# Optimization experiments

Hardware: AMD Instinct MI355X
Metric: run time of the kernel (lower is better)

Reference implementation:

```python
import jax, jax.numpy as jnp
import numpy as np

THRESH = 0.3
DECAY = 0.5


def spike_fn(x):
    # Heaviside threshold (forward only)
    return (x > THRESH).astype(x.dtype)


def setup_inputs() -> dict:
    key = jax.random.key(0)
    k_in, k0, k1, k2 = jax.random.split(key, 4)
    B, D0, T = 128, 512, 512
    inputs = jax.random.uniform(k_in, (B, D0, T), dtype=jnp.float32)
    w0 = jax.random.normal(k0, (512, 1024), dtype=jnp.float32)
    w1 = jax.random.normal(k1, (1024, 1024), dtype=jnp.float32)
    w2 = jax.random.normal(k2, (1024, 512), dtype=jnp.float32)
    return {"inputs": inputs, "w0": w0, "w1": w1, "w2": w2}


def reference(inputs, w0, w1, w2):
    ws = (w0, w1, w2)
    B = inputs.shape[0]
    layer_dims = tuple(w.shape[1] for w in ws)

    # time-major: [T, B, D0]
    xs = jnp.transpose(inputs, (2, 0, 1))

    mem0 = tuple(jnp.zeros((B, d), dtype=inputs.dtype) for d in layer_dims)
    spk0 = tuple(jnp.zeros((B, d), dtype=inputs.dtype) for d in layer_dims)

    def step(carry, x_t):
        mems, spikes = carry
        prev_spike = x_t  # layer-0 spikes come straight from the input
        new_mems, new_spikes = [], []
        for i, w in enumerate(ws):
            # leaky integrate with reset-by-spike, then fire
            mem = mems[i] * DECAY * (1.0 - spikes[i]) + prev_spike @ w
            s = spike_fn(mem)
            new_mems.append(mem)
            new_spikes.append(s)
            prev_spike = s
        return (tuple(new_mems), tuple(new_spikes)), None

    (_, spikes_final), _ = jax.lax.scan(step, (mem0, spk0), xs)
    return spikes_final[-1]
```

## Files before the change

kernel.cpp:

```cpp
#include <hip/hip_runtime.h>


typedef __bf16 bf16;
typedef __attribute__((ext_vector_type(8))) __bf16 bf16x8;
typedef __attribute__((ext_vector_type(16))) float f32x16;
typedef unsigned long long u64;

#define B_   128
#define D0_  512
#define T_   512
#define TS_  128
#define N1_  1024
#define N2_  1024
#define N3_  512
#define MFMA32(a,b,c) __builtin_amdgcn_mfma_f32_32x32x16_bf16((a),(b),(c),0,0,0)

#define GL2LDS(g, l) __builtin_amdgcn_global_load_lds( \
    (const __attribute__((address_space(1))) void*)(g), \
    (__attribute__((address_space(3))) void*)(l), 16, 0, 0)

#define WAIT_BARRIER() do { \
    asm volatile("s_waitcnt vmcnt(0)" ::: "memory"); \
    __builtin_amdgcn_s_barrier(); } while (0)


__global__ __launch_bounds__(256)
void split_w(const float* __restrict__ W, bf16* __restrict__ WTh, bf16* __restrict__ WTl,
             int K, int N)
{
    __shared__ float tile[32][33];
    const int k0 = blockIdx.x * 32, n0 = blockIdx.y * 32;
    const int tx = threadIdx.x & 31, ty = threadIdx.x >> 5;
#pragma unroll
    for (int r = 0; r < 4; ++r)
        tile[ty + r * 8][tx] = W[(size_t)(k0 + ty + r * 8) * N + n0 + tx];
    __syncthreads();
#pragma unroll
    for (int r = 0; r < 4; ++r) {
        int nl = ty + r * 8;
        float v = tile[tx][nl];
        bf16 h = (bf16)v;
        size_t o = (size_t)(n0 + nl) * K + k0 + tx;
        WTh[o] = h;
        WTl[o] = (bf16)(v - (float)h);
    }
}

__global__ __launch_bounds__(256)
void split_x(const float* __restrict__ in, bf16* __restrict__ Xh, bf16* __restrict__ Xl)
{
    __shared__ float tile[32][33];
    const int b = blockIdx.z, d0 = blockIdx.x * 32, t0 = blockIdx.y * 32;
    const int tx = threadIdx.x & 31, ty = threadIdx.x >> 5;
#pragma unroll
    for (int r = 0; r < 4; ++r)
        tile[ty + r * 8][tx] = in[((size_t)b * D0_ + d0 + ty + r * 8) * T_ + t0 + tx];
    __syncthreads();
    const int s = t0 >> 7;
#pragma unroll
    for (int r = 0; r < 4; ++r) {
        int t  = t0 + ty + r * 8;
        int tl = t & (TS_ - 1);
        float v = tile[tx][ty + r * 8];
        bf16 h = (bf16)v;
        size_t o = (((size_t)s * B_ + b) * TS_ + tl) * D0_ + d0 + tx;
        Xh[o] = h;
        Xl[o] = (bf16)(v - (float)h);
    }
}

__device__ __forceinline__ bf16x8 expand8(unsigned v)
{
    union { unsigned u[4]; bf16x8 h; } r;
    const unsigned p = v * 0x8001u;
#pragma unroll
    for (int i = 0; i < 4; ++i)
        r.u[i] = ((p >> (2 * i)) & 0x10001u) * 0x3F80u;
    return r.h;
}

__global__ __launch_bounds__(256, 2)
void snn_layer0(const bf16* __restrict__ Ah, const bf16* __restrict__ Al,
                const bf16* __restrict__ WTh, const bf16* __restrict__ WTl,
                u64* __restrict__ bitsOut)
{
    constexpr int K = D0_;
    __shared__ char smem[65536];
    bf16* sA0  = (bf16*)(smem);
    bf16* sAl0 = (bf16*)(smem + 8192);
    bf16* sB0  = (bf16*)(smem + 16384);
    bf16* sBl0 = (bf16*)(smem + 24576);
    bf16* sA1  = (bf16*)(smem + 32768);
    bf16* sAl1 = (bf16*)(smem + 40960);
    bf16* sB1  = (bf16*)(smem + 49152);
    bf16* sBl1 = (bf16*)(smem + 57344);
    float* If  = (float*)smem;

    const int tid = threadIdx.x, lane = tid & 63, w = tid >> 6;
    const int wm = w & 1, wn = w >> 1;
    const int l31 = lane & 31, kh = lane >> 5;
    const int b = blockIdx.x;
    const int nb = blockIdx.y * 128;

    const int i4 = lane >> 2, c4 = lane & 3;
    const int csrc = c4 ^ ((i4 >> 1) & 3);
    const bf16* gBh = WTh + (size_t)(nb + w * 32 + i4) * K + csrc * 8;
    const bf16* gBl = WTl + (size_t)(nb + w * 32 + i4) * K + csrc * 8;
    const int wT = w * 32 * 32;

    int rA[2], rB[2], swA[2], swB[2];
#pragma unroll
    for (int i = 0; i < 2; ++i) {
        rA[i] = wm * 64 + i * 32 + l31;
        rB[i] = wn * 64 + i * 32 + l31;
        swA[i] = (rA[i] >> 1) & 3;
        swB[i] = (rB[i] >> 1) & 3;
    }

    float cm = 0.f, cs = 0.f;
    const int scol = tid & 63;
    float* Ifb = If + (tid >> 6) * 4096;

#define STAGE0(dA, dAl, dBh, dBl, go)                                          \
    do {                                                                       \
        _Pragma("unroll")                                                      \
        for (int inst = 0; inst < 2; ++inst) {                                 \
            GL2LDS(gA  + (size_t)(inst * 16) * K + (go), (dA)  + wT + inst * 16 * 32); \
            GL2LDS(gAl + (size_t)(inst * 16) * K + (go), (dAl) + wT + inst * 16 * 32); \
            GL2LDS(gBh + (size_t)(inst * 16) * K + (go), (dBh) + wT + inst * 16 * 32); \
            GL2LDS(gBl + (size_t)(inst * 16) * K + (go), (dBl) + wT + inst * 16 * 32); \
        }                                                                      \
    } while (0)

#define KSTEP0(cA, cAl, cBh, cBl)                                              \
    do {                                                                       \
        bf16x8 a[2][2], al2[2][2];                                             \
        _Pragma("unroll")                                                      \
        for (int mi = 0; mi < 2; ++mi)                                         \
            _Pragma("unroll")                                                  \
            for (int h = 0; h < 2; ++h) {                                      \
                const int off = rA[mi] * 32 + (((2 * h + kh) ^ swA[mi]) * 8);  \
                a[mi][h]   = *(const bf16x8*)((cA) + off);                     \
                al2[mi][h] = *(const bf16x8*)((cAl) + off);                    \
            }                                                                  \
        _Pragma("unroll")                                                      \
        for (int ni = 0; ni < 2; ++ni) {                                       \
            _Pragma("unroll")                                                  \
            for (int h = 0; h < 2; ++h) {                                      \
                const int off = rB[ni] * 32 + (((2 * h + kh) ^ swB[ni]) * 8);  \
                bf16x8 bh = *(const bf16x8*)((cBh) + off);                     \
                bf16x8 bl = *(const bf16x8*)((cBl) + off);                     \
                _Pragma("unroll")                                              \
                for (int mi = 0; mi < 2; ++mi) {                               \
                    acc[mi][ni] = MFMA32(a[mi][h], bh, acc[mi][ni]);           \
                    acc[mi][ni] = MFMA32(al2[mi][h], bh, acc[mi][ni]);         \
                    acc[mi][ni] = MFMA32(a[mi][h], bl, acc[mi][ni]);           \
                }                                                              \
            }                                                                  \
        }                                                                      \
        WAIT_BARRIER();                                                        \
    } while (0)

#pragma unroll 1
    for (int s = 0; s < T_ / TS_; ++s) {
        const size_t arow = ((size_t)s * B_ + b) * TS_;
        const bf16* gA  = Ah + (arow + w * 32 + i4) * K + csrc * 8;
        const bf16* gAl = Al + (arow + w * 32 + i4) * K + csrc * 8;

        STAGE0(sA0, sAl0, sB0, sBl0, 0);
        WAIT_BARRIER();

        f32x16 acc[2][2] = {};

#pragma unroll 1
        for (int ks = 0; ks < K / 32; ks += 2) {
            STAGE0(sA1, sAl1, sB1, sBl1, (ks + 1) * 32);
            KSTEP0(sA0, sAl0, sB0, sBl0);
            if (ks + 2 < K / 32)
                STAGE0(sA0, sAl0, sB0, sBl0, (ks + 2) * 32);
            KSTEP0(sA1, sAl1, sB1, sBl1);
        }

        u64 word0 = 0, word1 = 0;
        if (wm == 0) {
#pragma unroll
            for (int ni = 0; ni < 2; ++ni)
#pragma unroll
                for (int mi = 0; mi < 2; ++mi)
#pragma unroll
                    for (int r = 0; r < 16; ++r) {
                        const int tt = mi * 32 + (r & 3) + 8 * (r >> 2) + 4 * kh;
                        If[wn * 4096 + tt * 64 + ni * 32 + l31] = acc[mi][ni][r];
                    }
        }
        __syncthreads();
        if (tid < 128) {
            float m = cm, sp = cs;
#pragma unroll 4
            for (int tt = 0; tt < 64; ++tt) {
                m = m * 0.5f * (1.0f - sp) + Ifb[tt * 64 + scol];
                const bool fire = m > 0.3f;
                sp = fire ? 1.0f : 0.0f;
                u64 bal = __ballot(fire);
                if ((tid & 63) == tt) word0 = bal;
            }
            cm = m; cs = sp;
        }
        __syncthreads();
        if (wm == 1) {
#pragma unroll
            for (int ni = 0; ni < 2; ++ni)
#pragma unroll
                for (int mi = 0; mi < 2; ++mi)
#pragma unroll
                    for (int r = 0; r < 16; ++r) {
                        const int tt = mi * 32 + (r & 3) + 8 * (r >> 2) + 4 * kh;
                        If[wn * 4096 + tt * 64 + ni * 32 + l31] = acc[mi][ni][r];
                    }
        }
        __syncthreads();
        if (tid < 128) {
            float m = cm, sp = cs;
#pragma unroll 4
            for (int tt = 0; tt < 64; ++tt) {
                m = m * 0.5f * (1.0f - sp) + Ifb[tt * 64 + scol];
                const bool fire = m > 0.3f;
                sp = fire ? 1.0f : 0.0f;
                u64 bal = __ballot(fire);
                if ((tid & 63) == tt) word1 = bal;
            }
            cm = m; cs = sp;
            u64* dst = bitsOut + ((size_t)s * B_ + b) * 2048;
            const int j8 = (nb >> 6) + (tid >> 6);
            const int t0 = tid & 63, t1 = 64 + (tid & 63);
            dst[t0 * 16 + (j8 ^ (t0 & 15))] = word0;
            dst[t1 * 16 + (j8 ^ (t1 & 15))] = word1;
        }
        __syncthreads();
    }
#undef STAGE0
#undef KSTEP0
}

template<bool WRITE_BITS>
__global__ __launch_bounds__(256, 2)
void snn_layer_bits(const u64* __restrict__ bitsIn,
                    const bf16* __restrict__ WTh, const bf16* __restrict__ WTl,
                    u64* __restrict__ bitsOut, float* __restrict__ outp, int N)
{
    constexpr int K = 1024;
    __shared__ char smem[81920];
    char* bitsLds = smem;
    bf16* sBh0 = (bf16*)(smem + 16384);
    bf16* sBl0 = (bf16*)(smem + 32768);
    bf16* sBh1 = (bf16*)(smem + 49152);
    bf16* sBl1 = (bf16*)(smem + 65536);
    float* If  = (float*)(smem + 16384);

    const int tid = threadIdx.x, lane = tid & 63, w = tid >> 6;
    const int wm = w & 1, wn = w >> 1;
    const int l31 = lane & 31, kh = lane >> 5;
    const int b = blockIdx.x;
    const int nb = blockIdx.y * 128;

    const int i8 = lane >> 3, c8 = lane & 7;
    const bf16* gBh = WTh + (size_t)(nb + w * 32 + i8) * K + (c8 ^ i8) * 8;
    const bf16* gBl = WTl + (size_t)(nb + w * 32 + i8) * K + (c8 ^ i8) * 8;
    const int wB = w * 32 * 64;

    int rA[2], rB[2];
#pragma unroll
    for (int i = 0; i < 2; ++i) {
        rA[i] = wm * 64 + i * 32 + l31;
        rB[i] = wn * 64 + i * 32 + l31;
    }
    const int sw7 = l31 & 7, sw15 = l31 & 15, sh8 = 8 * kh;

    float cm = 0.f, cs = 0.f;
    const int scol = tid & 63;
    float* Ifb = If + (tid >> 6) * 4096;

#define STAGEB(dBh, dBl, go)                                                   \
    do {                                                                       \
        _Pragma("unroll")                                                      \
        for (int inst = 0; inst < 4; ++inst) {                                 \
            GL2LDS(gBh + (size_t)(inst * 8) * K + (go), (dBh) + wB + inst * 8 * 64); \
            GL2LDS(gBl + (size_t)(inst * 8) * K + (go), (dBl) + wB + inst * 8 * 64); \
        }                                                                      \
    } while (0)

#define KSTEPB(ks, cBh, cBl)                                                   \
    do {                                                                       \
        u64 wA0 = *(const u64*)(bitsLds + rA[0] * 128 + (((ks) ^ sw15) << 3)) >> sh8; \
        u64 wA1 = *(const u64*)(bitsLds + rA[1] * 128 + (((ks) ^ sw15) << 3)) >> sh8; \
        _Pragma("unroll")                                                      \
        for (int h = 0; h < 4; ++h) {                                          \
            bf16x8 a0 = expand8((unsigned)(wA0 >> (16 * h)) & 0xFFu);          \
            bf16x8 a1 = expand8((unsigned)(wA1 >> (16 * h)) & 0xFFu);          \
            _Pragma("unroll")                                                  \
            for (int ni = 0; ni < 2; ++ni) {                                   \
                const int off = rB[ni] * 64 + (((2 * h + kh) ^ sw7) << 3);     \
                bf16x8 bh = *(const bf16x8*)((cBh) + off);                     \
                bf16x8 bl = *(const bf16x8*)((cBl) + off);                     \
                acc[0][ni] = MFMA32(a0, bh, acc[0][ni]);                       \
                acc[0][ni] = MFMA32(a0, bl, acc[0][ni]);                       \
                acc[1][ni] = MFMA32(a1, bh, acc[1][ni]);                       \
                acc[1][ni] = MFMA32(a1, bl, acc[1][ni]);                       \
            }                                                                  \
        }                                                                      \
        WAIT_BARRIER();                                                        \
    } while (0)

#pragma unroll 1
    for (int s = 0; s < T_ / TS_; ++s) {
        {
            const char* src = (const char*)bitsIn + ((size_t)s * B_ + b) * 16384;
#pragma unroll
            for (int i = 0; i < 4; ++i)
                GL2LDS(src + (w * 4 + i) * 1024 + lane * 16,
                       bitsLds + (w * 4 + i) * 1024);
        }
        STAGEB(sBh0, sBl0, 0);
        WAIT_BARRIER();

        f32x16 acc[2][2] = {};

#pragma unroll 1
        for (int ks = 0; ks < K / 64; ks += 2) {
            STAGEB(sBh1, sBl1, (ks + 1) * 64);
            KSTEPB(ks, sBh0, sBl0);
            if (ks + 2 < K / 64)
                STAGEB(sBh0, sBl0, (ks + 2) * 64);
            KSTEPB(ks + 1, sBh1, sBl1);
        }

        u64 word0 = 0, word1 = 0;
        if (wm == 0) {
#pragma unroll
            for (int ni = 0; ni < 2; ++ni)
#pragma unroll
                for (int mi = 0; mi < 2; ++mi)
#pragma unroll
                    for (int r = 0; r < 16; ++r) {
                        const int tt = mi * 32 + (r & 3) + 8 * (r >> 2) + 4 * kh;
                        If[wn * 4096 + tt * 64 + ni * 32 + l31] = acc[mi][ni][r];
                    }
        }
        __syncthreads();
        if (tid < 128) {
            float m = cm, sp = cs;
#pragma unroll 4
            for (int tt = 0; tt < 64; ++tt) {
                m = m * 0.5f * (1.0f - sp) + Ifb[tt * 64 + scol];
                const bool fire = m > 0.3f;
                sp = fire ? 1.0f : 0.0f;
                if constexpr (WRITE_BITS) {
                    u64 bal = __ballot(fire);
                    if ((tid & 63) == tt) word0 = bal;
                }
            }
            cm = m; cs = sp;
        }
        __syncthreads();
        if (wm == 1) {
#pragma unroll
            for (int ni = 0; ni < 2; ++ni)
#pragma unroll
                for (int mi = 0; mi < 2; ++mi)
#pragma unroll
                    for (int r = 0; r < 16; ++r) {
                        const int tt = mi * 32 + (r & 3) + 8 * (r >> 2) + 4 * kh;
                        If[wn * 4096 + tt * 64 + ni * 32 + l31] = acc[mi][ni][r];
                    }
        }
        __syncthreads();
        if (tid < 128) {
            float m = cm, sp = cs;
#pragma unroll 4
            for (int tt = 0; tt < 64; ++tt) {
                m = m * 0.5f * (1.0f - sp) + Ifb[tt * 64 + scol];
                const bool fire = m > 0.3f;
                sp = fire ? 1.0f : 0.0f;
                if constexpr (WRITE_BITS) {
                    u64 bal = __ballot(fire);
                    if ((tid & 63) == tt) word1 = bal;
                }
            }
            cm = m; cs = sp;
            if constexpr (WRITE_BITS) {
                u64* dst = bitsOut + ((size_t)s * B_ + b) * 2048;
                const int j8 = (nb >> 6) + (tid >> 6);
                const int t0 = tid & 63, t1 = 64 + (tid & 63);
                dst[t0 * 16 + (j8 ^ (t0 & 15))] = word0;
                dst[t1 * 16 + (j8 ^ (t1 & 15))] = word1;
            } else {
                if (s == T_ / TS_ - 1)
                    outp[(size_t)b * N + nb + tid] = cs;
            }
        }
        __syncthreads();
    }
#undef STAGEB
#undef KSTEPB
}

extern "C" void kernel_launch(void* const* d_in, const int* in_sizes, int n_in,
                              void* d_out, int out_size, void* d_ws, size_t ws_size,
                              hipStream_t stream)
{
    const float* x  = (const float*)d_in[0];
    const float* w0 = (const float*)d_in[1];
    const float* w1 = (const float*)d_in[2];
    const float* w2 = (const float*)d_in[3];
    float* out = (float*)d_out;

    char* p = (char*)d_ws;
    bf16* w0h = (bf16*)p;  p += (size_t)N1_ * D0_ * 2;
    bf16* w0l = (bf16*)p;  p += (size_t)N1_ * D0_ * 2;
    bf16* w1h = (bf16*)p;  p += (size_t)N2_ * N1_ * 2;
    bf16* w1l = (bf16*)p;  p += (size_t)N2_ * N1_ * 2;
    bf16* w2h = (bf16*)p;  p += (size_t)N3_ * N2_ * 2;
    bf16* w2l = (bf16*)p;  p += (size_t)N3_ * N2_ * 2;
    bf16* Xh  = (bf16*)p;  p += (size_t)T_ * B_ * D0_ * 2;
    bf16* Xl  = (bf16*)p;  p += (size_t)T_ * B_ * D0_ * 2;
    u64* bits0 = (u64*)p;  p += (size_t)(T_/TS_) * B_ * TS_ * (N1_/8);
    u64* bits1 = (u64*)p;  p += (size_t)(T_/TS_) * B_ * TS_ * (N2_/8);

    split_w<<<dim3(D0_/32, N1_/32), 256, 0, stream>>>(w0, w0h, w0l, D0_, N1_);
    split_w<<<dim3(N1_/32, N2_/32), 256, 0, stream>>>(w1, w1h, w1l, N1_, N2_);
    split_w<<<dim3(N2_/32, N3_/32), 256, 0, stream>>>(w2, w2h, w2l, N2_, N3_);
    split_x<<<dim3(D0_/32, T_/32, B_), 256, 0, stream>>>(x, Xh, Xl);

    snn_layer0<<<dim3(B_, N1_/128), 256, 0, stream>>>(Xh, Xl, w0h, w0l, bits0);
    snn_layer_bits<true ><<<dim3(B_, N2_/128), 256, 0, stream>>>(
        bits0, w1h, w1l, bits1, nullptr, N2_);
    snn_layer_bits<false><<<dim3(B_, N3_/128), 256, 0, stream>>>(
        bits1, w2h, w2l, nullptr, out, N3_);
}
```

Baseline: 804.2 us.

## Add wider 512-thread bit-spike layer kernel for the hidden layer

```diff
diff --git a/kernel.cpp b/kernel.cpp
--- a/kernel.cpp
+++ b/kernel.cpp
@@ -158,7 +158,7 @@
                 }                                                              \
             }                                                                  \
         }                                                                      \
-        WAIT_BARRIER();                                                        \
+        WAIT_BARRIER();                                                       \
     } while (0)
 
 #pragma unroll 1
@@ -308,7 +308,7 @@
                 acc[1][ni] = MFMA32(a1, bl, acc[1][ni]);                       \
             }                                                                  \
         }                                                                      \
-        WAIT_BARRIER();                                                        \
+        WAIT_BARRIER();                                                       \
     } while (0)
 
 #pragma unroll 1
@@ -404,6 +404,174 @@
 #undef KSTEPB
 }
 
+template<bool WRITE_BITS>
+__global__ __launch_bounds__(512, 4)
+void snn_layer_bits_wide(const u64* __restrict__ bitsIn,
+                         const bf16* __restrict__ WTh, const bf16* __restrict__ WTl,
+                         u64* __restrict__ bitsOut, float* __restrict__ outp, int N)
+{
+    constexpr int K = 1024;
+    __shared__ char smem[65536];
+    char* bitsLds = smem;
+    bf16* sBh = (bf16*)(smem + 16384);
+    bf16* sBl = (bf16*)(smem + 32768);
+    float* If = (float*)smem;
+
+    const int tid = threadIdx.x, lane = tid & 63, w = tid >> 6;
+    const int wm = w & 1, wn = w >> 1;
+    const int l31 = lane & 31, kh = lane >> 5;
+    const int b = blockIdx.x;
+    const int nb = blockIdx.y * 256;
+
+    const int i4 = lane >> 2, c4 = lane & 3;
+    const int csrc = c4 ^ ((i4 >> 1) & 3);
+    const bf16* gBh0 = WTh + (size_t)(nb + w * 16 + i4) * K + csrc * 8;
+    const bf16* gBh1 = WTh + (size_t)(nb + 128 + w * 16 + i4) * K + csrc * 8;
+    const bf16* gBl0 = WTl + (size_t)(nb + w * 16 + i4) * K + csrc * 8;
+    const bf16* gBl1 = WTl + (size_t)(nb + 128 + w * 16 + i4) * K + csrc * 8;
+    const int dB0 = (w * 16) * 32;
+    const int dB1 = (128 + w * 16) * 32;
+
+    int rA[2], rB[2], swB[2];
+#pragma unroll
+    for (int i = 0; i < 2; ++i) {
+        rA[i] = wm * 64 + i * 32 + l31;
+        rB[i] = wn * 64 + i * 32 + l31;
+        swB[i] = (rB[i] >> 1) & 3;
+    }
+    const int sh8 = 8 * kh;
+    const int bA0 = rA[0] * 128, bA1 = rA[1] * 128;
+    const int s15a = rA[0] & 15, s15b = rA[1] & 15;
+
+    float cm = 0.f, cs = 0.f;
+
+#define STAGEW(go)                                                             \
+    do {                                                                       \
+        GL2LDS(gBh0 + (go), sBh + dB0);                                        \
+        GL2LDS(gBh1 + (go), sBh + dB1);                                        \
+        GL2LDS(gBl0 + (go), sBl + dB0);                                        \
+        GL2LDS(gBl1 + (go), sBl + dB1);                                        \
+    } while (0)
+
+#define KSTEPW(wa0, wa1)                                                       \
+    do {                                                                       \
+        _Pragma("unroll")                                                      \
+        for (int h = 0; h < 2; ++h) {                                          \
+            bf16x8 a0 = expand8(((wa0) >> (16 * h + sh8)) & 0xFFu);            \
+            bf16x8 a1 = expand8(((wa1) >> (16 * h + sh8)) & 0xFFu);            \
+            _Pragma("unroll")                                                  \
+            for (int ni = 0; ni < 2; ++ni) {                                   \
+                const int off = rB[ni] * 32 + (((2 * h + kh) ^ swB[ni]) * 8);  \
+                bf16x8 bh = *(const bf16x8*)(sBh + off);                       \
+                bf16x8 bl = *(const bf16x8*)(sBl + off);                       \
+                acc[0][ni] = MFMA32(a0, bh, acc[0][ni]);                       \
+                acc[0][ni] = MFMA32(a0, bl, acc[0][ni]);                       \
+                acc[1][ni] = MFMA32(a1, bh, acc[1][ni]);                       \
+                acc[1][ni] = MFMA32(a1, bl, acc[1][ni]);                       \
+            }                                                                  \
+        }                                                                      \
+    } while (0)
+
+#pragma unroll 1
+    for (int s = 0; s < T_ / TS_; ++s) {
+        {
+            const char* src = (const char*)bitsIn + ((size_t)s * B_ + b) * 16384;
+            GL2LDS(src + w * 2048 + lane * 16, bitsLds + w * 2048);
+            GL2LDS(src + w * 2048 + 1024 + lane * 16, bitsLds + w * 2048 + 1024);
+        }
+        STAGEW(0);
+        WAIT_BARRIER();
+
+        f32x16 acc[2][2] = {};
+
+#pragma unroll 1
+        for (int ks = 0; ks < K / 32; ks += 2) {
+            const int j8 = ks >> 1;
+            const u64 w0 = *(const u64*)(bitsLds + bA0 + ((j8 ^ s15a) << 3));
+            const u64 w1 = *(const u64*)(bitsLds + bA1 + ((j8 ^ s15b) << 3));
+
+            KSTEPW((unsigned)w0, (unsigned)w1);
+            __builtin_amdgcn_s_barrier();
+            STAGEW((ks + 1) * 32);
+            WAIT_BARRIER();
+
+            KSTEPW((unsigned)(w0 >> 32), (unsigned)(w1 >> 32));
+            __builtin_amdgcn_s_barrier();
+            if (ks + 2 < K / 32)
+                STAGEW((ks + 2) * 32);
+            WAIT_BARRIER();
+        }
+
+        u64 word0 = 0, word1 = 0;
+        if (wm == 0) {
+#pragma unroll
+            for (int ni = 0; ni < 2; ++ni)
+#pragma unroll
+                for (int mi = 0; mi < 2; ++mi)
+#pragma unroll
+                    for (int r = 0; r < 16; ++r) {
+                        const int tt = mi * 32 + (r & 3) + 8 * (r >> 2) + 4 * kh;
+                        If[tt * 256 + wn * 64 + ni * 32 + l31] = acc[mi][ni][r];
+                    }
+        }
+        __syncthreads();
+        if (tid < 256) {
+            float m = cm, sp = cs;
+#pragma unroll 4
+            for (int tt = 0; tt < 64; ++tt) {
+                m = m * 0.5f * (1.0f - sp) + If[tt * 256 + tid];
+                const bool fire = m > 0.3f;
+                sp = fire ? 1.0f : 0.0f;
+                if constexpr (WRITE_BITS) {
+                    u64 bal = __ballot(fire);
+                    if ((tid & 63) == tt) word0 = bal;
+                }
+            }
+            cm = m; cs = sp;
+        }
+        __syncthreads();
+        if (wm == 1) {
+#pragma unroll
+            for (int ni = 0; ni < 2; ++ni)
+#pragma unroll
+                for (int mi = 0; mi < 2; ++mi)
+#pragma unroll
+                    for (int r = 0; r < 16; ++r) {
+                        const int tt = mi * 32 + (r & 3) + 8 * (r >> 2) + 4 * kh;
+                        If[tt * 256 + wn * 64 + ni * 32 + l31] = acc[mi][ni][r];
+                    }
+        }
+        __syncthreads();
+        if (tid < 256) {
+            float m = cm, sp = cs;
+#pragma unroll 4
+            for (int tt = 0; tt < 64; ++tt) {
+                m = m * 0.5f * (1.0f - sp) + If[tt * 256 + tid];
+                const bool fire = m > 0.3f;
+                sp = fire ? 1.0f : 0.0f;
+                if constexpr (WRITE_BITS) {
+                    u64 bal = __ballot(fire);
+                    if ((tid & 63) == tt) word1 = bal;
+                }
+            }
+            cm = m; cs = sp;
+            if constexpr (WRITE_BITS) {
+                u64* dst = bitsOut + ((size_t)s * B_ + b) * 2048;
+                const int j8 = (nb >> 6) + (tid >> 6);
+                const int t0 = tid & 63, t1 = 64 + (tid & 63);
+                dst[t0 * 16 + (j8 ^ (t0 & 15))] = word0;
+                dst[t1 * 16 + (j8 ^ (t1 & 15))] = word1;
+            } else {
+                if (s == T_ / TS_ - 1)
+                    outp[(size_t)b * N + nb + tid] = cs;
+            }
+        }
+        __syncthreads();
+    }
+#undef STAGEW
+#undef KSTEPW
+}
+
 extern "C" void kernel_launch(void* const* d_in, const int* in_sizes, int n_in,
                               void* d_out, int out_size, void* d_ws, size_t ws_size,
                               hipStream_t stream)
@@ -432,7 +600,7 @@
     split_x<<<dim3(D0_/32, T_/32, B_), 256, 0, stream>>>(x, Xh, Xl);
 
     snn_layer0<<<dim3(B_, N1_/128), 256, 0, stream>>>(Xh, Xl, w0h, w0l, bits0);
-    snn_layer_bits<true ><<<dim3(B_, N2_/128), 256, 0, stream>>>(
+    snn_layer_bits_wide<true><<<dim3(B_, N2_/256), 512, 0, stream>>>(
         bits0, w1h, w1l, bits1, nullptr, N2_);
     snn_layer_bits<false><<<dim3(B_, N3_/128), 256, 0, stream>>>(
         bits1, w2h, w2l, nullptr, out, N3_);
```

Result: no change. 814.0 us (+1.2%).

## Use 4-stage K=32 weight pipeline with partial vmcnt waits and MFMA priority

Applied to the files above, without the earlier changes.

```diff
diff --git a/kernel.cpp b/kernel.cpp
--- a/kernel.cpp
+++ b/kernel.cpp
@@ -143,6 +143,7 @@
                 a[mi][h]   = *(const bf16x8*)((cA) + off);                     \
                 al2[mi][h] = *(const bf16x8*)((cAl) + off);                    \
             }                                                                  \
+        __builtin_amdgcn_s_setprio(1);                                         \
         _Pragma("unroll")                                                      \
         for (int ni = 0; ni < 2; ++ni) {                                       \
             _Pragma("unroll")                                                  \
@@ -158,6 +159,7 @@
                 }                                                              \
             }                                                                  \
         }                                                                      \
+        __builtin_amdgcn_s_setprio(0);                                         \
         WAIT_BARRIER();                                                        \
     } while (0)
 
@@ -251,11 +253,10 @@
     constexpr int K = 1024;
     __shared__ char smem[81920];
     char* bitsLds = smem;
-    bf16* sBh0 = (bf16*)(smem + 16384);
-    bf16* sBl0 = (bf16*)(smem + 32768);
-    bf16* sBh1 = (bf16*)(smem + 49152);
-    bf16* sBl1 = (bf16*)(smem + 65536);
-    float* If  = (float*)(smem + 16384);
+    float* If = (float*)(smem + 16384);
+
+#define SBUF_H(j) ((bf16*)(smem + 16384 + (j) * 16384))
+#define SBUF_L(j) ((bf16*)(smem + 16384 + (j) * 16384 + 8192))
 
     const int tid = threadIdx.x, lane = tid & 63, w = tid >> 6;
     const int wm = w & 1, wn = w >> 1;
@@ -263,52 +264,66 @@
     const int b = blockIdx.x;
     const int nb = blockIdx.y * 128;
 
-    const int i8 = lane >> 3, c8 = lane & 7;
-    const bf16* gBh = WTh + (size_t)(nb + w * 32 + i8) * K + (c8 ^ i8) * 8;
-    const bf16* gBl = WTl + (size_t)(nb + w * 32 + i8) * K + (c8 ^ i8) * 8;
-    const int wB = w * 32 * 64;
-
-    int rA[2], rB[2];
+    const int i4 = lane >> 2, c4 = lane & 3;
+    const int csrc = c4 ^ ((i4 >> 1) & 3);
+    const bf16* gBh = WTh + (size_t)(nb + w * 32 + i4) * K + csrc * 8;
+    const bf16* gBl = WTl + (size_t)(nb + w * 32 + i4) * K + csrc * 8;
+    const int wOff = (w * 32) * 32;
+
+    int rA[2], rB[2], swB[2];
 #pragma unroll
     for (int i = 0; i < 2; ++i) {
         rA[i] = wm * 64 + i * 32 + l31;
         rB[i] = wn * 64 + i * 32 + l31;
-    }
-    const int sw7 = l31 & 7, sw15 = l31 & 15, sh8 = 8 * kh;
+        swB[i] = (rB[i] >> 1) & 3;
+    }
+    const int sh8 = 8 * kh;
+    const int bA0 = rA[0] * 128, bA1 = rA[1] * 128;
+    const int s15a = rA[0] & 15, s15b = rA[1] & 15;
 
     float cm = 0.f, cs = 0.f;
     const int scol = tid & 63;
     float* Ifb = If + (tid >> 6) * 4096;
 
-#define STAGEB(dBh, dBl, go)                                                   \
+#define STAGEN(j, go)                                                          \
+    do {                                                                       \
+        GL2LDS(gBh + (size_t)(go),              SBUF_H(j) + wOff);             \
+        GL2LDS(gBh + (size_t)16 * K + (go),     SBUF_H(j) + wOff + 512);       \
+        GL2LDS(gBl + (size_t)(go),              SBUF_L(j) + wOff);             \
+        GL2LDS(gBl + (size_t)16 * K + (go),     SBUF_L(j) + wOff + 512);       \
+    } while (0)
+
+#define KSTEPN(j, x0, x1)                                                      \
     do {                                                                       \
         _Pragma("unroll")                                                      \
-        for (int inst = 0; inst < 4; ++inst) {                                 \
-            GL2LDS(gBh + (size_t)(inst * 8) * K + (go), (dBh) + wB + inst * 8 * 64); \
-            GL2LDS(gBl + (size_t)(inst * 8) * K + (go), (dBl) + wB + inst * 8 * 64); \
-        }                                                                      \
-    } while (0)
-
-#define KSTEPB(ks, cBh, cBl)                                                   \
-    do {                                                                       \
-        u64 wA0 = *(const u64*)(bitsLds + rA[0] * 128 + (((ks) ^ sw15) << 3)) >> sh8; \
-        u64 wA1 = *(const u64*)(bitsLds + rA[1] * 128 + (((ks) ^ sw15) << 3)) >> sh8; \
-        _Pragma("unroll")                                                      \
-        for (int h = 0; h < 4; ++h) {                                          \
-            bf16x8 a0 = expand8((unsigned)(wA0 >> (16 * h)) & 0xFFu);          \
-            bf16x8 a1 = expand8((unsigned)(wA1 >> (16 * h)) & 0xFFu);          \
+        for (int h = 0; h < 2; ++h) {                                          \
+            bf16x8 a0 = expand8(((x0) >> (16 * h + sh8)) & 0xFFu);             \
+            bf16x8 a1 = expand8(((x1) >> (16 * h + sh8)) & 0xFFu);             \
+            __builtin_amdgcn_s_setprio(1);                                     \
             _Pragma("unroll")                                                  \
             for (int ni = 0; ni < 2; ++ni) {                                   \
-                const int off = rB[ni] * 64 + (((2 * h + kh) ^ sw7) << 3);     \
-                bf16x8 bh = *(const bf16x8*)((cBh) + off);                     \
-                bf16x8 bl = *(const bf16x8*)((cBl) + off);                     \
+                const int off = rB[ni] * 32 + (((2 * h + kh) ^ swB[ni]) * 8);  \
+                bf16x8 bh = *(const bf16x8*)(SBUF_H(j) + off);                 \
+                bf16x8 bl = *(const bf16x8*)(SBUF_L(j) + off);                 \
                 acc[0][ni] = MFMA32(a0, bh, acc[0][ni]);                       \
                 acc[0][ni] = MFMA32(a0, bl, acc[0][ni]);                       \
                 acc[1][ni] = MFMA32(a1, bh, acc[1][ni]);                       \
                 acc[1][ni] = MFMA32(a1, bl, acc[1][ni]);                       \
             }                                                                  \
+            __builtin_amdgcn_s_setprio(0);                                     \
         }                                                                      \
-        WAIT_BARRIER();                                                        \
+    } while (0)
+
+#define STEPN(ks, bufj, issj, DOISS, VMN)                                      \
+    do {                                                                       \
+        asm volatile("s_waitcnt vmcnt(" VMN ")" ::: "memory");                 \
+        __builtin_amdgcn_s_barrier();                                          \
+        if (DOISS) STAGEN(issj, ((ks) + 3) * 32);                              \
+        const u64 wa0_ = *(const u64*)(bitsLds + bA0 + ((((ks) >> 1) ^ s15a) << 3)); \
+        const u64 wa1_ = *(const u64*)(bitsLds + bA1 + ((((ks) >> 1) ^ s15b) << 3)); \
+        const unsigned x0_ = (unsigned)(wa0_ >> (32 * ((ks) & 1)));            \
+        const unsigned x1_ = (unsigned)(wa1_ >> (32 * ((ks) & 1)));            \
+        KSTEPN(bufj, x0_, x1_);                                                \
     } while (0)
 
 #pragma unroll 1
@@ -320,19 +335,23 @@
                 GL2LDS(src + (w * 4 + i) * 1024 + lane * 16,
                        bitsLds + (w * 4 + i) * 1024);
         }
-        STAGEB(sBh0, sBl0, 0);
-        WAIT_BARRIER();
+        STAGEN(0, 0);
+        STAGEN(1, 32);
+        STAGEN(2, 64);
 
         f32x16 acc[2][2] = {};
 
 #pragma unroll 1
-        for (int ks = 0; ks < K / 64; ks += 2) {
-            STAGEB(sBh1, sBl1, (ks + 1) * 64);
-            KSTEPB(ks, sBh0, sBl0);
-            if (ks + 2 < K / 64)
-                STAGEB(sBh0, sBl0, (ks + 2) * 64);
-            KSTEPB(ks + 1, sBh1, sBl1);
-        }
+        for (int base = 0; base < 28; base += 4) {
+            STEPN(base + 0, 0, 3, true, "8");
+            STEPN(base + 1, 1, 0, true, "8");
+            STEPN(base + 2, 2, 1, true, "8");
+            STEPN(base + 3, 3, 2, true, "8");
+        }
+        STEPN(28, 0, 3, true,  "8");
+        STEPN(29, 1, 0, false, "8");
+        STEPN(30, 2, 0, false, "4");
+        STEPN(31, 3, 0, false, "0");
 
         u64 word0 = 0, word1 = 0;
         if (wm == 0) {
@@ -400,8 +419,11 @@
         }
         __syncthreads();
     }
-#undef STAGEB
-#undef KSTEPB
+#undef STAGEN
+#undef KSTEPN
+#undef STEPN
+#undef SBUF_H
+#undef SBUF_L
 }
 
 extern "C" void kernel_launch(void* const* d_in, const int* in_sizes, int n_in,
```

Result: slower. 837.3 us (+4.1%).
